# Kernel optimization log

Measured on AMD Instinct MI355X. Metric: run time of the kernel, lower is better.

## Reference

```python
import jax, jax.numpy as jnp
import numpy as np

T_VALUES = (2.0, 8.0, 32.0, 128.0)
EPS = 1e-05
N_BANDS = 128


def setup_inputs() -> dict:
    key = jax.random.key(0)
    k1, k2, k3, k4 = jax.random.split(key, 4)
    x = jax.random.uniform(k1, (8, N_BANDS, 8192), dtype=jnp.float32)
    # Parameters are stored in log-space, matching the torch module's init
    # (log(alpha), log(delta), log(r) broadcast to n_bands).
    log_alpha = jnp.full((N_BANDS,), np.log(0.8), dtype=jnp.float32)
    log_delta = jnp.full((N_BANDS,), np.log(10.0), dtype=jnp.float32)
    log_r = jnp.full((N_BANDS,), np.log(0.25), dtype=jnp.float32)
    return {"x": x, "log_alpha": log_alpha, "log_delta": log_delta, "log_r": log_r}


def reference(x, log_alpha, log_delta, log_r):
    # x: [B, F, N]  (batch, bands, time frames)
    t_vals = jnp.asarray(T_VALUES, dtype=x.dtype)
    # s = (sqrt(1 + 4 t^2) - 1) / (2 t^2)  -- smoothing coefficient per rate
    s_vals = (jnp.sqrt(1.0 + 4.0 * t_vals ** 2) - 1.0) / (2.0 * t_vals ** 2)

    alpha = jnp.exp(log_alpha)[:, None]  # [F, 1]
    delta = jnp.exp(log_delta)[:, None]
    r = jnp.exp(log_r)[:, None]

    xt = jnp.moveaxis(x, -1, 0)  # [N, B, F], scan over time

    def ema(s):
        # IIR recursion m[t] = s*x[t] + (1-s)*m[t-1], m[-1] = x[0].
        # This is exactly what the torch triangular-matmul formulation computes:
        # smoother[t] = s * sum_{i<=t} x[i] (1-s)^{t-i} + (1-s)^{t+1} x[0].
        def step(m, xi):
            m = s * xi + (1.0 - s) * m
            return m, m
        _, ys = jax.lax.scan(step, xt[0], xt)
        return jnp.moveaxis(ys, 0, -1)  # [B, F, N]

    smoother = jax.vmap(ema)(s_vals)  # [T, B, F, N]

    # smooth = (eps + smoother)^(-alpha), written as in the source via log1p
    smooth = jnp.exp(-alpha * (jnp.log(EPS) + jnp.log1p(smoother / EPS)))
    pcen = (x[None] * smooth + delta) ** r - delta ** r  # [T, B, F, N]
    return jnp.transpose(pcen, (1, 0, 2, 3))  # [B, T, F, N]
```

## Files before the change

kernel.cpp:

```cpp
#include <hip/hip_runtime.h>

#define NB    128
#define NT    8192
#define TPB   256
#define CHUNK 32

__device__ __forceinline__ int swz(int n) { return n ^ (((n >> 5) & 7) << 2); }

__global__ __launch_bounds__(TPB, 4) void mrpcen_kernel(
    const float* __restrict__ x,
    const float* __restrict__ log_alpha,
    const float* __restrict__ log_delta,
    const float* __restrict__ log_r,
    float* __restrict__ out)
{
    __shared__ __align__(16) float sh[NT];
    __shared__ float4 sB4[TPB];

    const int tid = threadIdx.x;
    const int bf  = blockIdx.x;
    const int b   = bf >> 7;
    const int f   = bf & (NB - 1);

    const float* xrow = x + (size_t)bf * NT;

    const float alpha  = __expf(log_alpha[f]);
    const float r      = __expf(log_r[f]);
    const float delta  = __expf(log_delta[f]);
    const float deltar = __expf(r * log_delta[f]);

    float s[4], A[4];
    const float tv[4] = {2.f, 8.f, 32.f, 128.f};
#pragma unroll
    for (int t = 0; t < 4; t++) {
        float t2 = tv[t] * tv[t];
        s[t] = (sqrtf(1.f + 4.f * t2) - 1.f) / (2.f * t2);
        float a1 = 1.f - s[t];
        float a = a1 * a1; a = a * a; a = a * a; a = a * a; a = a * a;
        A[t] = a;
    }

#pragma unroll
    for (int k = 0; k < 8; k++) {
        int n = k * 1024 + tid * 4;
        float4 v = *reinterpret_cast<const float4*>(xrow + n);
        *reinterpret_cast<float4*>(&sh[swz(n)]) = v;
    }
    __syncthreads();

    const float x0 = sh[0];

    float xc[CHUNK];
#pragma unroll
    for (int j = 0; j < 8; j++) {
        int n = tid * CHUNK + 4 * j;
        float4 v = *reinterpret_cast<const float4*>(&sh[swz(n)]);
        xc[4 * j + 0] = v.x; xc[4 * j + 1] = v.y;
        xc[4 * j + 2] = v.z; xc[4 * j + 3] = v.w;
    }

    float Bl[4] = {0.f, 0.f, 0.f, 0.f};
#pragma unroll
    for (int i = 0; i < CHUNK; i++) {
        float xi = xc[i];
#pragma unroll
        for (int t = 0; t < 4; t++)
            Bl[t] = s[t] * xi + (1.f - s[t]) * Bl[t];
    }

    sB4[tid] = make_float4(Bl[0], Bl[1], Bl[2], Bl[3]);
    float ap0 = A[0], ap1 = A[1], ap2 = A[2], ap3 = A[3];
    for (int d = 1; d < TPB; d <<= 1) {
        __syncthreads();
        float4 cur = sB4[tid];
        float4 prev = make_float4(0.f, 0.f, 0.f, 0.f);
        if (tid >= d) prev = sB4[tid - d];
        __syncthreads();
        if (tid >= d) {
            cur.x += ap0 * prev.x;
            cur.y += ap1 * prev.y;
            cur.z += ap2 * prev.z;
            cur.w += ap3 * prev.w;
            sB4[tid] = cur;
        }
        ap0 *= ap0; ap1 *= ap1; ap2 *= ap2; ap3 *= ap3;
    }
    __syncthreads();
    float4 Sp = (tid > 0) ? sB4[tid - 1] : make_float4(0.f, 0.f, 0.f, 0.f);
    const float Sprev[4] = {Sp.x, Sp.y, Sp.z, Sp.w};

    float m_in[4];
#pragma unroll
    for (int t = 0; t < 4; t++) {
        float p = 1.f, base = A[t];
        int e = tid;
#pragma unroll
        for (int bit = 0; bit < 8; bit++) {
            if (e & 1) p *= base;
            base *= base;
            e >>= 1;
        }
        m_in[t] = p * x0 + Sprev[t];
    }

    for (int t = 0; t < 4; t++) {
        const float st = s[t], a1 = 1.f - s[t];
        float m = m_in[t];
#pragma unroll
        for (int j = 0; j < 8; j++) {
            float ov[4];
#pragma unroll
            for (int q = 0; q < 4; q++) {
                float xi = xc[4 * j + q];
                m = st * xi + a1 * m;
                float smooth = __expf(-alpha * __logf(1e-5f + m));
                ov[q] = __expf(r * __logf(xi * smooth + delta)) - deltar;
            }
            float4 o = make_float4(ov[0], ov[1], ov[2], ov[3]);
            *reinterpret_cast<float4*>(&sh[swz(tid * CHUNK + 4 * j)]) = o;
        }
        __syncthreads();
        float* oplane = out + (((size_t)b * 4 + t) * NB + f) * (size_t)NT;
#pragma unroll
        for (int k = 0; k < 8; k++) {
            int n = k * 1024 + tid * 4;
            float4 v = *reinterpret_cast<const float4*>(&sh[swz(n)]);
            *reinterpret_cast<float4*>(oplane + n) = v;
        }
        __syncthreads();
    }
}

extern "C" void kernel_launch(void* const* d_in, const int* in_sizes, int n_in,
                              void* d_out, int out_size, void* d_ws, size_t ws_size,
                              hipStream_t stream) {
    const float* x         = (const float*)d_in[0];
    const float* log_alpha = (const float*)d_in[1];
    const float* log_delta = (const float*)d_in[2];
    const float* log_r     = (const float*)d_in[3];
    float* out = (float*)d_out;

    mrpcen_kernel<<<dim3(8 * NB), dim3(TPB), 0, stream>>>(
        x, log_alpha, log_delta, log_r, out);
}
```

Baseline: 187.9 us.

## Replace LDS block scan with wavefront shuffle scan and direct global IO

```diff
diff --git a/kernel.cpp b/kernel.cpp
--- a/kernel.cpp
+++ b/kernel.cpp
@@ -1,26 +1,26 @@
 #include <hip/hip_runtime.h>
 
-#define NB    128
-#define NT    8192
-#define TPB   256
-#define CHUNK 32
+#define NB  128
+#define NT  8192
+#define TPB 512
+#define PT  16
+#define NW  (TPB / 64)
 
-__device__ __forceinline__ int swz(int n) { return n ^ (((n >> 5) & 7) << 2); }
-
-__global__ __launch_bounds__(TPB, 4) void mrpcen_kernel(
+__global__ __launch_bounds__(TPB, 8) void mrpcen_kernel(
     const float* __restrict__ x,
     const float* __restrict__ log_alpha,
     const float* __restrict__ log_delta,
     const float* __restrict__ log_r,
     float* __restrict__ out)
 {
-    __shared__ __align__(16) float sh[NT];
-    __shared__ float4 sB4[TPB];
+    __shared__ float4 wtot[NW];
 
-    const int tid = threadIdx.x;
-    const int bf  = blockIdx.x;
-    const int b   = bf >> 7;
-    const int f   = bf & (NB - 1);
+    const int tid  = threadIdx.x;
+    const int lane = tid & 63;
+    const int wv   = tid >> 6;
+    const int bf   = blockIdx.x;
+    const int b    = bf >> 7;
+    const int f    = bf & (NB - 1);
 
     const float* xrow = x + (size_t)bf * NT;
 
@@ -29,85 +29,96 @@
     const float delta  = __expf(log_delta[f]);
     const float deltar = __expf(r * log_delta[f]);
 
-    float s[4], A[4];
+    float s[4], A16[4];
     const float tv[4] = {2.f, 8.f, 32.f, 128.f};
 #pragma unroll
     for (int t = 0; t < 4; t++) {
         float t2 = tv[t] * tv[t];
         s[t] = (sqrtf(1.f + 4.f * t2) - 1.f) / (2.f * t2);
-        float a1 = 1.f - s[t];
-        float a = a1 * a1; a = a * a; a = a * a; a = a * a; a = a * a;
-        A[t] = a;
+        float a = 1.f - s[t];
+        a = a * a; a = a * a; a = a * a; a = a * a;
+        A16[t] = a;
     }
 
+    float xc[PT];
+    const float4* xv = reinterpret_cast<const float4*>(xrow + tid * PT);
 #pragma unroll
-    for (int k = 0; k < 8; k++) {
-        int n = k * 1024 + tid * 4;
-        float4 v = *reinterpret_cast<const float4*>(xrow + n);
-        *reinterpret_cast<float4*>(&sh[swz(n)]) = v;
-    }
-    __syncthreads();
-
-    const float x0 = sh[0];
-
-    float xc[CHUNK];
-#pragma unroll
-    for (int j = 0; j < 8; j++) {
-        int n = tid * CHUNK + 4 * j;
-        float4 v = *reinterpret_cast<const float4*>(&sh[swz(n)]);
+    for (int j = 0; j < 4; j++) {
+        float4 v = xv[j];
         xc[4 * j + 0] = v.x; xc[4 * j + 1] = v.y;
         xc[4 * j + 2] = v.z; xc[4 * j + 3] = v.w;
     }
+    const float m0 = xrow[0];
 
-    float Bl[4] = {0.f, 0.f, 0.f, 0.f};
+    float B[4] = {0.f, 0.f, 0.f, 0.f};
 #pragma unroll
-    for (int i = 0; i < CHUNK; i++) {
+    for (int i = 0; i < PT; i++) {
         float xi = xc[i];
 #pragma unroll
         for (int t = 0; t < 4; t++)
-            Bl[t] = s[t] * xi + (1.f - s[t]) * Bl[t];
+            B[t] = s[t] * xi + (1.f - s[t]) * B[t];
     }
 
-    sB4[tid] = make_float4(Bl[0], Bl[1], Bl[2], Bl[3]);
-    float ap0 = A[0], ap1 = A[1], ap2 = A[2], ap3 = A[3];
-    for (int d = 1; d < TPB; d <<= 1) {
-        __syncthreads();
-        float4 cur = sB4[tid];
-        float4 prev = make_float4(0.f, 0.f, 0.f, 0.f);
-        if (tid >= d) prev = sB4[tid - d];
-        __syncthreads();
-        if (tid >= d) {
-            cur.x += ap0 * prev.x;
-            cur.y += ap1 * prev.y;
-            cur.z += ap2 * prev.z;
-            cur.w += ap3 * prev.w;
-            sB4[tid] = cur;
+    float S[4] = {B[0], B[1], B[2], B[3]};
+    float F[4] = {A16[0], A16[1], A16[2], A16[3]};
+#pragma unroll
+    for (int d = 1; d < 64; d <<= 1) {
+#pragma unroll
+        for (int t = 0; t < 4; t++) {
+            float up = __shfl_up(S[t], d, 64);
+            up = (lane >= d) ? up : 0.f;
+            S[t] += F[t] * up;
+            F[t] *= F[t];
         }
-        ap0 *= ap0; ap1 *= ap1; ap2 *= ap2; ap3 *= ap3;
     }
+
+    if (lane == 63) wtot[wv] = make_float4(S[0], S[1], S[2], S[3]);
     __syncthreads();
-    float4 Sp = (tid > 0) ? sB4[tid - 1] : make_float4(0.f, 0.f, 0.f, 0.f);
-    const float Sprev[4] = {Sp.x, Sp.y, Sp.z, Sp.w};
 
-    float m_in[4];
+    float A1024[4];
 #pragma unroll
     for (int t = 0; t < 4; t++) {
-        float p = 1.f, base = A[t];
-        int e = tid;
+        float a = A16[t];
+        a = a * a; a = a * a; a = a * a; a = a * a; a = a * a; a = a * a;
+        A1024[t] = a;
+    }
+
+    float P[4]  = {0.f, 0.f, 0.f, 0.f};
+    float Ap[4] = {1.f, 1.f, 1.f, 1.f};
+    for (int w = 0; w < wv; w++) {
+        float4 W = wtot[w];
+        P[0] = W.x + A1024[0] * P[0];
+        P[1] = W.y + A1024[1] * P[1];
+        P[2] = W.z + A1024[2] * P[2];
+        P[3] = W.w + A1024[3] * P[3];
 #pragma unroll
-        for (int bit = 0; bit < 8; bit++) {
+        for (int t = 0; t < 4; t++) Ap[t] *= A1024[t];
+    }
+
+    float mtin[4];
+#pragma unroll
+    for (int t = 0; t < 4; t++) {
+        float sp = __shfl_up(S[t], 1, 64);
+        sp = lane ? sp : 0.f;
+        float p = 1.f, base = A16[t];
+        int e = lane;
+#pragma unroll
+        for (int bit = 0; bit < 6; bit++) {
             if (e & 1) p *= base;
             base *= base;
             e >>= 1;
         }
-        m_in[t] = p * x0 + Sprev[t];
+        float mwave = Ap[t] * m0 + P[t];
+        mtin[t] = p * mwave + sp;
     }
 
+#pragma unroll
     for (int t = 0; t < 4; t++) {
         const float st = s[t], a1 = 1.f - s[t];
-        float m = m_in[t];
+        float m = mtin[t];
+        float* op = out + (((size_t)b * 4 + t) * NB + f) * (size_t)NT + tid * PT;
 #pragma unroll
-        for (int j = 0; j < 8; j++) {
+        for (int j = 0; j < 4; j++) {
             float ov[4];
 #pragma unroll
             for (int q = 0; q < 4; q++) {
@@ -116,18 +127,8 @@
                 float smooth = __expf(-alpha * __logf(1e-5f + m));
                 ov[q] = __expf(r * __logf(xi * smooth + delta)) - deltar;
             }
-            float4 o = make_float4(ov[0], ov[1], ov[2], ov[3]);
-            *reinterpret_cast<float4*>(&sh[swz(tid * CHUNK + 4 * j)]) = o;
+            reinterpret_cast<float4*>(op)[j] = make_float4(ov[0], ov[1], ov[2], ov[3]);
         }
-        __syncthreads();
-        float* oplane = out + (((size_t)b * 4 + t) * NB + f) * (size_t)NT;
-#pragma unroll
-        for (int k = 0; k < 8; k++) {
-            int n = k * 1024 + tid * 4;
-            float4 v = *reinterpret_cast<const float4*>(&sh[swz(n)]);
-            *reinterpret_cast<float4*>(oplane + n) = v;
-        }
-        __syncthreads();
     }
 }
 
```

Measured after the change: 248.9 us. +32.5%, slower.
